# Kernel tuning notes

Hardware: AMD Instinct MI355X
Metric: run time of the kernel (lower is better)

The kernel has to match this reference:

```python
import jax, jax.numpy as jnp
import numpy as np

B, N, T, E = 8, 1024, 16, 512
H = 8                      # heads
DH = E // H                # head_dim = 64
KNN = 16                   # knn_k (N-1 > 16 so k = 16)
L = 4                      # time_window (<= T)
TAU_MIN = 1e-4
BIAS_SCALE = 1.0


def setup_inputs() -> dict:
    key = jax.random.key(0)
    ks = jax.random.split(key, 12)
    hidden = jax.random.normal(ks[0], (B, N, T, E), jnp.float32)
    positions_xy = jax.random.uniform(ks[1], (N, 2), jnp.float32) * 100.0
    s = 1.0 / np.sqrt(E)
    Wq = jax.random.normal(ks[2], (E, E), jnp.float32) * s
    bq = jnp.zeros((E,), jnp.float32)
    Wk = jax.random.normal(ks[3], (E, E), jnp.float32) * s
    bk = jnp.zeros((E,), jnp.float32)
    Wv = jax.random.normal(ks[4], (E, E), jnp.float32) * s
    bv = jnp.zeros((E,), jnp.float32)
    Wo = jax.random.normal(ks[5], (E, E), jnp.float32) * s
    bo = jnp.zeros((E,), jnp.float32)
    tau = jnp.asarray(1.0, jnp.float32)
    return {"hidden": hidden, "positions_xy": positions_xy,
            "Wq": Wq, "bq": bq, "Wk": Wk, "bk": bk,
            "Wv": Wv, "bv": bv, "Wo": Wo, "bo": bo, "tau": tau}


def reference(hidden, positions_xy, Wq, bq, Wk, bk, Wv, bv, Wo, bo, tau):
    b, n, t, e = hidden.shape
    # --- kNN over static positions (no_grad in the original) ---
    pos = jax.lax.stop_gradient(positions_xy)
    x2 = jnp.sum(pos * pos, axis=1, keepdims=True)          # [N,1]
    d2 = jnp.clip(x2 + x2.T - 2.0 * (pos @ pos.T), 0.0)
    D = jnp.sqrt(d2 + 1e-9)
    D = D + jnp.diag(jnp.full((n,), jnp.inf, D.dtype))       # exclude self
    neg_d, knn_idx = jax.lax.top_k(-D, KNN)                  # smallest-k
    knn_dists = -neg_d                                        # [N,K]

    h_last = hidden[:, :, -1, :]                              # [B,N,E]
    # mean over last L steps, then gather neighbors (== gather-then-mean)
    neigh_mean = jnp.mean(hidden[:, :, -L:, :], axis=2)       # [B,N,E]
    neigh_repr = neigh_mean[:, knn_idx]                       # [B,N,K,E]

    # --- distance bias ---
    eps = jnp.finfo(hidden.dtype).eps
    local_scale = jnp.maximum(jnp.mean(knn_dists, axis=1, keepdims=True), eps)
    d_hat = knn_dists / local_scale                           # [N,K]
    tau_safe = jnp.maximum(tau, TAU_MIN)
    log_w = jnp.clip(BIAS_SCALE * (-d_hat / tau_safe), -10.0, 0.0)

    # --- distance-biased multi-head attention over k neighbors ---
    Q = (h_last @ Wq.T + bq).reshape(b, n, H, DH)             # [B,N,H,Dh]
    K = (neigh_repr @ Wk.T + bk).reshape(b, n, KNN, H, DH)    # [B,N,K,H,Dh]
    V = (neigh_repr @ Wv.T + bv).reshape(b, n, KNN, H, DH)
    logits = jnp.einsum('bnhd,bnkhd->bnhk', Q, K) / jnp.sqrt(jnp.asarray(DH, hidden.dtype))
    logits = logits + log_w[None, :, None, :]                 # [B,N,H,K]
    attn = jax.nn.softmax(logits, axis=-1)                    # dropout=0 (eval)
    ctx = jnp.einsum('bnhk,bnkhd->bnhd', attn, V).reshape(b, n, H * DH)
    return ctx @ Wo.T + bo                                    # [B,N,E]
```

## Files before the change

### kernel.cpp

```cpp
#include <hip/hip_runtime.h>
#include <math.h>

#define B_   8
#define N_   1024
#define T_   16
#define E_   512
#define H_   8
#define DH_  64
#define KNN_ 16

typedef __attribute__((ext_vector_type(8))) _Float16 half8;
typedef __attribute__((ext_vector_type(2))) _Float16 half2v;
typedef __attribute__((ext_vector_type(4))) float    f32x4;

__global__ __launch_bounds__(256) void knn_kernel(const float* __restrict__ pos,
                                                  const float* __restrict__ tau_p,
                                                  int* __restrict__ knn_idx,
                                                  float* __restrict__ logw) {
    __shared__ float dist[N_];
    __shared__ float rval[4];
    __shared__ int   ridx[4];
    __shared__ float sel_d[KNN_];
    __shared__ int   sel_i[KNN_];

    const int i = blockIdx.x;
    const int t = threadIdx.x;

    const float px = pos[2 * i], py = pos[2 * i + 1];
    const float xi2 = px * px + py * py;

    for (int j = t; j < N_; j += 256) {
        const float qx = pos[2 * j], qy = pos[2 * j + 1];
        const float xj2 = qx * qx + qy * qy;
        float d2 = xi2 + xj2 - 2.0f * (px * qx + py * qy);
        d2 = fmaxf(d2, 0.0f);
        const float d = sqrtf(d2 + 1e-9f);
        dist[j] = (j == i) ? __builtin_inff() : d;
    }
    __syncthreads();

    for (int k = 0; k < KNN_; ++k) {
        float best = __builtin_inff();
        int bi = 0x7fffffff;
        for (int j = t; j < N_; j += 256) {
            const float d = dist[j];
            if (d < best) { best = d; bi = j; }
        }
        for (int off = 32; off >= 1; off >>= 1) {
            const float ov = __shfl_down(best, off);
            const int   oi = __shfl_down(bi, off);
            if (ov < best || (ov == best && oi < bi)) { best = ov; bi = oi; }
        }
        const int wave = t >> 6;
        if ((t & 63) == 0) { rval[wave] = best; ridx[wave] = bi; }
        __syncthreads();
        if (t == 0) {
            for (int w = 1; w < 4; ++w) {
                if (rval[w] < best || (rval[w] == best && ridx[w] < bi)) { best = rval[w]; bi = ridx[w]; }
            }
            sel_d[k] = best;
            sel_i[k] = bi;
            dist[bi] = __builtin_inff();
        }
        __syncthreads();
    }

    if (t < KNN_) {
        float mean = 0.0f;
        for (int k = 0; k < KNN_; ++k) mean += sel_d[k];
        mean *= (1.0f / KNN_);
        const float scale = fmaxf(mean, 1.1920929e-7f);
        const float tau_safe = fmaxf(tau_p[0], 1e-4f);
        float lw = -(sel_d[t] / scale) / tau_safe;
        lw = fminf(fmaxf(lw, -10.0f), 0.0f);
        logw[i * KNN_ + t]    = lw;
        knn_idx[i * KNN_ + t] = sel_i[t];
    }
}

__global__ __launch_bounds__(256) void last_mean_kernel(const float* __restrict__ hidden,
                                                        float* __restrict__ h_last,
                                                        float* __restrict__ neigh_mean) {
    const int idx = blockIdx.x * 256 + threadIdx.x;
    const int e4 = idx & (E_ / 4 - 1);
    const int bn = idx >> 7;
    const float4* h = (const float4*)hidden;
    const size_t base = (size_t)bn * (T_ * (E_ / 4)) + e4;
    const float4 a = h[base + 12 * (E_ / 4)];
    const float4 b = h[base + 13 * (E_ / 4)];
    const float4 c = h[base + 14 * (E_ / 4)];
    const float4 d = h[base + 15 * (E_ / 4)];
    ((float4*)h_last)[idx] = d;
    float4 m;
    m.x = (a.x + b.x + c.x + d.x) * 0.25f;
    m.y = (a.y + b.y + c.y + d.y) * 0.25f;
    m.z = (a.z + b.z + c.z + d.z) * 0.25f;
    m.w = (a.w + b.w + c.w + d.w) * 0.25f;
    ((float4*)neigh_mean)[idx] = m;
}

__device__ __forceinline__ void split_store(unsigned short* __restrict__ Hs,
                                            unsigned short* __restrict__ Ls,
                                            int byt, float4 v) {
    union { _Float16 h[4]; uint2 u; } Hu, Lu;
    const float* f = (const float*)&v;
#pragma unroll
    for (int j = 0; j < 4; ++j) {
        const _Float16 hh = (_Float16)f[j];
        Hu.h[j] = hh;
        Lu.h[j] = (_Float16)(f[j] - (float)hh);
    }
    *(uint2*)((char*)Hs + byt) = Hu.u;
    *(uint2*)((char*)Ls + byt) = Lu.u;
}

template <typename OT>
__device__ __forceinline__ void gemm_split_f16(const float* __restrict__ A,
                                               const float* __restrict__ Wt,
                                               const float* __restrict__ bias,
                                               OT* __restrict__ C) {
    __shared__ unsigned short AhS[128 * 64];
    __shared__ unsigned short AlS[128 * 64];
    __shared__ unsigned short WhS[128 * 64];
    __shared__ unsigned short WlS[128 * 64];

    const int t    = threadIdx.x;
    const int m0   = blockIdx.x * 128;
    const int j0   = blockIdx.y * 128;
    const int lane = t & 63;
    const int wv   = t >> 6;
    const int wm   = wv >> 1;
    const int wn   = wv & 1;
    const int lr   = lane & 15;
    const int kg   = lane >> 4;

    float4 ra[8], rw[8];
#pragma unroll
    for (int s = 0; s < 8; ++s) {
        const int f4 = s * 256 + t;
        const int row = f4 >> 4, k4 = f4 & 15;
        ra[s] = *(const float4*)(A  + (size_t)(m0 + row) * 512 + k4 * 4);
        rw[s] = *(const float4*)(Wt + (size_t)(j0 + row) * 512 + k4 * 4);
    }

    f32x4 acc[4][4];
    const f32x4 zero = {0.0f, 0.0f, 0.0f, 0.0f};
#pragma unroll
    for (int f = 0; f < 4; ++f)
#pragma unroll
        for (int g = 0; g < 4; ++g) acc[f][g] = zero;

    for (int it = 0; it < 8; ++it) {
        __syncthreads();
#pragma unroll
        for (int s = 0; s < 8; ++s) {
            const int f4 = s * 256 + t;
            const int row = f4 >> 4, k4 = f4 & 15;
            const int byt = (row << 7) + ((k4 * 8) ^ ((row & 7) << 4));
            split_store(AhS, AlS, byt, ra[s]);
            split_store(WhS, WlS, byt, rw[s]);
        }
        __syncthreads();
        if (it < 7) {
            const int kc = (it + 1) * 64;
#pragma unroll
            for (int s = 0; s < 8; ++s) {
                const int f4 = s * 256 + t;
                const int row = f4 >> 4, k4 = f4 & 15;
                ra[s] = *(const float4*)(A  + (size_t)(m0 + row) * 512 + kc + k4 * 4);
                rw[s] = *(const float4*)(Wt + (size_t)(j0 + row) * 512 + kc + k4 * 4);
            }
        }
#pragma unroll
        for (int ks = 0; ks < 2; ++ks) {
            half8 ah[4], al[4], wh[4], wl[4];
#pragma unroll
            for (int f = 0; f < 4; ++f) {
                const int row = wm * 64 + f * 16 + lr;
                const int byt = (row << 7) + (((ks * 64) + (kg * 16)) ^ ((row & 7) << 4));
                ah[f] = *(const half8*)((const char*)AhS + byt);
                al[f] = *(const half8*)((const char*)AlS + byt);
            }
#pragma unroll
            for (int g = 0; g < 4; ++g) {
                const int row = wn * 64 + g * 16 + lr;
                const int byt = (row << 7) + (((ks * 64) + (kg * 16)) ^ ((row & 7) << 4));
                wh[g] = *(const half8*)((const char*)WhS + byt);
                wl[g] = *(const half8*)((const char*)WlS + byt);
            }
#pragma unroll
            for (int f = 0; f < 4; ++f)
#pragma unroll
                for (int g = 0; g < 4; ++g)
                    acc[f][g] = __builtin_amdgcn_mfma_f32_16x16x32_f16(ah[f], wh[g], acc[f][g], 0, 0, 0);
#pragma unroll
            for (int f = 0; f < 4; ++f)
#pragma unroll
                for (int g = 0; g < 4; ++g)
                    acc[f][g] = __builtin_amdgcn_mfma_f32_16x16x32_f16(ah[f], wl[g], acc[f][g], 0, 0, 0);
#pragma unroll
            for (int f = 0; f < 4; ++f)
#pragma unroll
                for (int g = 0; g < 4; ++g)
                    acc[f][g] = __builtin_amdgcn_mfma_f32_16x16x32_f16(al[f], wh[g], acc[f][g], 0, 0, 0);
        }
    }

#pragma unroll
    for (int g = 0; g < 4; ++g) {
        const int n  = j0 + wn * 64 + g * 16 + lr;
        const float bn = bias[n];
#pragma unroll
        for (int f = 0; f < 4; ++f) {
            const int mrow = m0 + wm * 64 + f * 16 + kg * 4;
#pragma unroll
            for (int q = 0; q < 4; ++q)
                C[(size_t)(mrow + q) * 512 + n] = (OT)(acc[f][g][q] + bn);
        }
    }
}

__global__ __launch_bounds__(256, 2) void qkv_gemm_kernel(const float* __restrict__ h_last,
                                                          const float* __restrict__ nmean,
                                                          const float* __restrict__ Wq,
                                                          const float* __restrict__ Wk,
                                                          const float* __restrict__ Wv,
                                                          const float* __restrict__ bq,
                                                          const float* __restrict__ bk,
                                                          const float* __restrict__ bv,
                                                          float* __restrict__ Qo,
                                                          _Float16* __restrict__ Ko,
                                                          _Float16* __restrict__ Vo) {
    const int which = blockIdx.z;
    if (which == 0) {
        gemm_split_f16<float>(h_last, Wq, bq, Qo);
    } else if (which == 1) {
        gemm_split_f16<_Float16>(nmean, Wk, bk, Ko);
    } else {
        gemm_split_f16<_Float16>(nmean, Wv, bv, Vo);
    }
}

__global__ __launch_bounds__(256, 2) void out_gemm_kernel(const float* __restrict__ ctx,
                                                          const float* __restrict__ Wo,
                                                          const float* __restrict__ bo,
                                                          float* __restrict__ out) {
    gemm_split_f16<float>(ctx, Wo, bo, out);
}

__global__ __launch_bounds__(256) void attn_kernel(const float* __restrict__ Q,
                                                   const _Float16* __restrict__ Kf,
                                                   const _Float16* __restrict__ Vf,
                                                   const int* __restrict__ knn_idx,
                                                   const float* __restrict__ logw,
                                                   float* __restrict__ ctx) {
    const int bid = blockIdx.x;
    const int bn  = ((bid & 7) << 10) | (bid >> 3);
    const int n   = bn & (N_ - 1);
    const int b   = bn >> 10;
    const int t   = threadIdx.x;

    __shared__ int   idxs[KNN_];
    __shared__ float lws[KNN_];
    if (t < KNN_) {
        idxs[t] = knn_idx[n * KNN_ + t];
        lws[t]  = logw[n * KNN_ + t];
    }
    __syncthreads();

    const float2 q = ((const float2*)Q)[(size_t)bn * 256 + t];

    float logits[KNN_];
#pragma unroll
    for (int k = 0; k < KNN_; ++k) {
        const int j = idxs[k];
        const half2v kv = ((const half2v*)Kf)[((size_t)(b * N_ + j)) * 256 + t];
        float d = q.x * (float)kv.x + q.y * (float)kv.y;
        d += __shfl_xor(d, 1);
        d += __shfl_xor(d, 2);
        d += __shfl_xor(d, 4);
        d += __shfl_xor(d, 8);
        d += __shfl_xor(d, 16);
        logits[k] = d * 0.125f + lws[k];
    }

    float m = -__builtin_inff();
#pragma unroll
    for (int k = 0; k < KNN_; ++k) m = fmaxf(m, logits[k]);
    float p[KNN_];
    float s = 0.0f;
#pragma unroll
    for (int k = 0; k < KNN_; ++k) { p[k] = expf(logits[k] - m); s += p[k]; }
    const float inv = 1.0f / s;

    float2 acc = make_float2(0.0f, 0.0f);
#pragma unroll
    for (int k = 0; k < KNN_; ++k) {
        const int j = idxs[k];
        const half2v vv = ((const half2v*)Vf)[((size_t)(b * N_ + j)) * 256 + t];
        const float w = p[k] * inv;
        acc.x = fmaf(w, (float)vv.x, acc.x);
        acc.y = fmaf(w, (float)vv.y, acc.y);
    }
    ((float2*)ctx)[(size_t)bn * 256 + t] = acc;
}

extern "C" void kernel_launch(void* const* d_in, const int* in_sizes, int n_in,
                              void* d_out, int out_size, void* d_ws, size_t ws_size,
                              hipStream_t stream) {
    const float* hidden = (const float*)d_in[0];
    const float* pos    = (const float*)d_in[1];
    const float* Wq     = (const float*)d_in[2];
    const float* bq     = (const float*)d_in[3];
    const float* Wk     = (const float*)d_in[4];
    const float* bk     = (const float*)d_in[5];
    const float* Wv     = (const float*)d_in[6];
    const float* bv     = (const float*)d_in[7];
    const float* Wo     = (const float*)d_in[8];
    const float* bo     = (const float*)d_in[9];
    const float* tau    = (const float*)d_in[10];

    float* ws      = (float*)d_ws;
    const size_t SZ = (size_t)B_ * N_ * E_;
    float*    h_last  = ws;
    float*    nmean   = ws + SZ;
    _Float16* Kh      = (_Float16*)(ws + 2 * SZ);
    _Float16* Vh      = (_Float16*)(ws + 2 * SZ + SZ / 2);
    int*      knn_idx = (int*)(ws + 3 * SZ);
    float*    logw    = ws + 3 * SZ + N_ * KNN_;
    float*    Qb      = (float*)d_out;
    float*    out     = (float*)d_out;

    knn_kernel<<<N_, 256, 0, stream>>>(pos, tau, knn_idx, logw);
    last_mean_kernel<<<(B_ * N_ * E_ / 4) / 256, 256, 0, stream>>>(hidden, h_last, nmean);

    dim3 gqkv(B_ * N_ / 128, E_ / 128, 3);
    qkv_gemm_kernel<<<gqkv, 256, 0, stream>>>(h_last, nmean, Wq, Wk, Wv, bq, bk, bv, Qb, Kh, Vh);

    attn_kernel<<<B_ * N_, 256, 0, stream>>>(Qb, Kh, Vh, knn_idx, logw, h_last );

    dim3 gout(B_ * N_ / 128, E_ / 128, 1);
    out_gemm_kernel<<<gout, 256, 0, stream>>>(h_last, Wo, bo, out);
}
```

Before: 478.9 us.

## Pre-split weights to fp16 hi/lo and stream GEMM tiles via global_load_lds

Adds a kernel that splits all four weight matrices into fp16 hi/lo halves once per call. The last-step and mean activations are now stored as single fp16, which lets the QKV GEMM drop the lo-activation MFMA pass (2 passes instead of 3). Q is stored in fp16, and the attention output is written as an fp16 hi/lo pair for a 3-pass output GEMM. Both GEMMs now load tiles directly into LDS with global_load_lds and no register staging, conversion or swizzle. This removes the per-tile fp32-to-fp16 split work and halves activation traffic, at the cost of lower precision for the activations and Q, possible LDS bank conflicts without the swizzle, and no register prefetch overlap.

Result: faster. 441.8 us (-7.8%).

```diff
diff --git a/kernel.cpp b/kernel.cpp
--- a/kernel.cpp
+++ b/kernel.cpp
@@ -10,6 +10,7 @@
 #define KNN_ 16
 
 typedef __attribute__((ext_vector_type(8))) _Float16 half8;
+typedef __attribute__((ext_vector_type(4))) _Float16 half4;
 typedef __attribute__((ext_vector_type(2))) _Float16 half2v;
 typedef __attribute__((ext_vector_type(4))) float    f32x4;
 
@@ -78,9 +79,32 @@
     }
 }
 
+__global__ __launch_bounds__(256) void wsplit_kernel(const float* __restrict__ Wq,
+                                                     const float* __restrict__ Wk,
+                                                     const float* __restrict__ Wv,
+                                                     const float* __restrict__ Wo,
+                                                     _Float16* __restrict__ dst) {
+    const int id  = blockIdx.x * 256 + threadIdx.x;
+    const int mat = id >> 16;
+    const int i   = id & 65535;
+    const float* src = (mat == 0) ? Wq : (mat == 1) ? Wk : (mat == 2) ? Wv : Wo;
+    const float4 v = ((const float4*)src)[i];
+    half4 hi, lo;
+    const float* f = (const float*)&v;
+#pragma unroll
+    for (int j = 0; j < 4; ++j) {
+        const _Float16 hh = (_Float16)f[j];
+        hi[j] = hh;
+        lo[j] = (_Float16)(f[j] - (float)hh);
+    }
+    _Float16* dh = dst + (size_t)mat * 2 * 262144;
+    *(half4*)(dh + (size_t)i * 4)          = hi;
+    *(half4*)(dh + 262144 + (size_t)i * 4) = lo;
+}
+
 __global__ __launch_bounds__(256) void last_mean_kernel(const float* __restrict__ hidden,
-                                                        float* __restrict__ h_last,
-                                                        float* __restrict__ neigh_mean) {
+                                                        _Float16* __restrict__ hlast_h,
+                                                        _Float16* __restrict__ nmean_h) {
     const int idx = blockIdx.x * 256 + threadIdx.x;
     const int e4 = idx & (E_ / 4 - 1);
     const int bn = idx >> 7;
@@ -90,58 +114,44 @@
     const float4 b = h[base + 13 * (E_ / 4)];
     const float4 c = h[base + 14 * (E_ / 4)];
     const float4 d = h[base + 15 * (E_ / 4)];
-    ((float4*)h_last)[idx] = d;
-    float4 m;
-    m.x = (a.x + b.x + c.x + d.x) * 0.25f;
-    m.y = (a.y + b.y + c.y + d.y) * 0.25f;
-    m.z = (a.z + b.z + c.z + d.z) * 0.25f;
-    m.w = (a.w + b.w + c.w + d.w) * 0.25f;
-    ((float4*)neigh_mean)[idx] = m;
-}
-
-__device__ __forceinline__ void split_store(unsigned short* __restrict__ Hs,
-                                            unsigned short* __restrict__ Ls,
-                                            int byt, float4 v) {
-    union { _Float16 h[4]; uint2 u; } Hu, Lu;
-    const float* f = (const float*)&v;
+    half4 hl, nm;
+    const float* df = (const float*)&d;
+    const float* af = (const float*)&a;
+    const float* bf = (const float*)&b;
+    const float* cf = (const float*)&c;
 #pragma unroll
     for (int j = 0; j < 4; ++j) {
-        const _Float16 hh = (_Float16)f[j];
-        Hu.h[j] = hh;
-        Lu.h[j] = (_Float16)(f[j] - (float)hh);
-    }
-    *(uint2*)((char*)Hs + byt) = Hu.u;
-    *(uint2*)((char*)Ls + byt) = Lu.u;
-}
-
-template <typename OT>
-__device__ __forceinline__ void gemm_split_f16(const float* __restrict__ A,
-                                               const float* __restrict__ Wt,
-                                               const float* __restrict__ bias,
-                                               OT* __restrict__ C) {
-    __shared__ unsigned short AhS[128 * 64];
-    __shared__ unsigned short AlS[128 * 64];
-    __shared__ unsigned short WhS[128 * 64];
-    __shared__ unsigned short WlS[128 * 64];
+        hl[j] = (_Float16)df[j];
+        nm[j] = (_Float16)((af[j] + bf[j] + cf[j] + df[j]) * 0.25f);
+    }
+    *(half4*)(hlast_h + (size_t)idx * 4) = hl;
+    *(half4*)(nmean_h + (size_t)idx * 4) = nm;
+}
+
+__device__ __forceinline__ void gload16(const void* g, void* l) {
+    __builtin_amdgcn_global_load_lds((const __attribute__((address_space(1))) void*)g,
+                                     (__attribute__((address_space(3))) void*)l, 16, 0, 0);
+}
+
+template <int PASSES, typename OT>
+__device__ __forceinline__ void gemm_f16(const _Float16* __restrict__ Ah,
+                                         const _Float16* __restrict__ Al,
+                                         const _Float16* __restrict__ Wh,
+                                         const _Float16* __restrict__ Wl,
+                                         const float* __restrict__ bias,
+                                         OT* __restrict__ C) {
+    constexpr int NARR  = (PASSES == 3) ? 4 : 3;
+    constexpr int WHOFF = (PASSES == 3) ? 32768 : 16384;
+    __shared__ unsigned short lds[NARR * 8192];
 
     const int t    = threadIdx.x;
     const int m0   = blockIdx.x * 128;
     const int j0   = blockIdx.y * 128;
     const int lane = t & 63;
     const int wv   = t >> 6;
-    const int wm   = wv >> 1;
-    const int wn   = wv & 1;
-    const int lr   = lane & 15;
-    const int kg   = lane >> 4;
-
-    float4 ra[8], rw[8];
-#pragma unroll
-    for (int s = 0; s < 8; ++s) {
-        const int f4 = s * 256 + t;
-        const int row = f4 >> 4, k4 = f4 & 15;
-        ra[s] = *(const float4*)(A  + (size_t)(m0 + row) * 512 + k4 * 4);
-        rw[s] = *(const float4*)(Wt + (size_t)(j0 + row) * 512 + k4 * 4);
-    }
+    const int wm   = wv >> 1, wn = wv & 1;
+    const int lr   = lane & 15, kg = lane >> 4;
+    const int lsub = (lane >> 3) * 1024 + (lane & 7) * 16;
 
     f32x4 acc[4][4];
     const f32x4 zero = {0.0f, 0.0f, 0.0f, 0.0f};
@@ -151,42 +161,39 @@
         for (int g = 0; g < 4; ++g) acc[f][g] = zero;
 
     for (int it = 0; it < 8; ++it) {
+        const size_t kb = (size_t)(it * 64) * 2;
+        const char* gA  = (const char*)Ah + (size_t)m0 * 1024 + kb;
+        const char* gWh = (const char*)Wh + (size_t)j0 * 1024 + kb;
+        const char* gWl = (const char*)Wl + (size_t)j0 * 1024 + kb;
+        const char* gAl = (PASSES == 3) ? (const char*)Al + (size_t)m0 * 1024 + kb : (const char*)0;
+#pragma unroll
+        for (int jj = 0; jj < NARR * 4; ++jj) {
+            const int j = wv * (NARR * 4) + jj;
+            const int arr = j >> 4, slab = j & 15;
+            const char* gb;
+            if (PASSES == 3)
+                gb = (arr == 0) ? gA : (arr == 1) ? gAl : (arr == 2) ? gWh : gWl;
+            else
+                gb = (arr == 0) ? gA : (arr == 1) ? gWh : gWl;
+            gload16(gb + (size_t)slab * 8192 + lsub, (char*)lds + j * 1024);
+        }
         __syncthreads();
-#pragma unroll
-        for (int s = 0; s < 8; ++s) {
-            const int f4 = s * 256 + t;
-            const int row = f4 >> 4, k4 = f4 & 15;
-            const int byt = (row << 7) + ((k4 * 8) ^ ((row & 7) << 4));
-            split_store(AhS, AlS, byt, ra[s]);
-            split_store(WhS, WlS, byt, rw[s]);
-        }
-        __syncthreads();
-        if (it < 7) {
-            const int kc = (it + 1) * 64;
-#pragma unroll
-            for (int s = 0; s < 8; ++s) {
-                const int f4 = s * 256 + t;
-                const int row = f4 >> 4, k4 = f4 & 15;
-                ra[s] = *(const float4*)(A  + (size_t)(m0 + row) * 512 + kc + k4 * 4);
-                rw[s] = *(const float4*)(Wt + (size_t)(j0 + row) * 512 + kc + k4 * 4);
+
+#pragma unroll
+        for (int ks = 0; ks < 2; ++ks) {
+            const int ko = ks * 64 + kg * 16;
+            half8 ah[4], al[4], wh[4], wl[4];
+#pragma unroll
+            for (int f = 0; f < 4; ++f) {
+                const int abyt = (wm * 64 + f * 16 + lr) * 128 + ko;
+                ah[f] = *(const half8*)((const char*)lds + abyt);
+                if (PASSES == 3) al[f] = *(const half8*)((const char*)lds + 16384 + abyt);
             }
-        }
-#pragma unroll
-        for (int ks = 0; ks < 2; ++ks) {
-            half8 ah[4], al[4], wh[4], wl[4];
-#pragma unroll
-            for (int f = 0; f < 4; ++f) {
-                const int row = wm * 64 + f * 16 + lr;
-                const int byt = (row << 7) + (((ks * 64) + (kg * 16)) ^ ((row & 7) << 4));
-                ah[f] = *(const half8*)((const char*)AhS + byt);
-                al[f] = *(const half8*)((const char*)AlS + byt);
-            }
 #pragma unroll
             for (int g = 0; g < 4; ++g) {
-                const int row = wn * 64 + g * 16 + lr;
-                const int byt = (row << 7) + (((ks * 64) + (kg * 16)) ^ ((row & 7) << 4));
-                wh[g] = *(const half8*)((const char*)WhS + byt);
-                wl[g] = *(const half8*)((const char*)WlS + byt);
+                const int wbyt = (wn * 64 + g * 16 + lr) * 128 + ko;
+                wh[g] = *(const half8*)((const char*)lds + WHOFF + wbyt);
+                wl[g] = *(const half8*)((const char*)lds + WHOFF + 16384 + wbyt);
             }
 #pragma unroll
             for (int f = 0; f < 4; ++f)
@@ -198,62 +205,66 @@
 #pragma unroll
                 for (int g = 0; g < 4; ++g)
                     acc[f][g] = __builtin_amdgcn_mfma_f32_16x16x32_f16(ah[f], wl[g], acc[f][g], 0, 0, 0);
-#pragma unroll
-            for (int f = 0; f < 4; ++f)
-#pragma unroll
-                for (int g = 0; g < 4; ++g)
-                    acc[f][g] = __builtin_amdgcn_mfma_f32_16x16x32_f16(al[f], wh[g], acc[f][g], 0, 0, 0);
-        }
+            if (PASSES == 3) {
+#pragma unroll
+                for (int f = 0; f < 4; ++f)
+#pragma unroll
+                    for (int g = 0; g < 4; ++g)
+                        acc[f][g] = __builtin_amdgcn_mfma_f32_16x16x32_f16(al[f], wh[g], acc[f][g], 0, 0, 0);
+            }
+        }
+        if (it < 7) __syncthreads();
     }
 
 #pragma unroll
     for (int g = 0; g < 4; ++g) {
-        const int n  = j0 + wn * 64 + g * 16 + lr;
-        const float bn = bias[n];
+        const int n = j0 + wn * 64 + g * 16 + lr;
+        const float bn_ = bias[n];
 #pragma unroll
         for (int f = 0; f < 4; ++f) {
             const int mrow = m0 + wm * 64 + f * 16 + kg * 4;
 #pragma unroll
             for (int q = 0; q < 4; ++q)
-                C[(size_t)(mrow + q) * 512 + n] = (OT)(acc[f][g][q] + bn);
-        }
-    }
-}
-
-__global__ __launch_bounds__(256, 2) void qkv_gemm_kernel(const float* __restrict__ h_last,
-                                                          const float* __restrict__ nmean,
-                                                          const float* __restrict__ Wq,
-                                                          const float* __restrict__ Wk,
-                                                          const float* __restrict__ Wv,
+                C[(size_t)(mrow + q) * 512 + n] = (OT)(acc[f][g][q] + bn_);
+        }
+    }
+}
+
+__global__ __launch_bounds__(256, 3) void qkv_gemm_kernel(const _Float16* __restrict__ hlast_h,
+                                                          const _Float16* __restrict__ nmean_h,
+                                                          const _Float16* __restrict__ Wsp,
                                                           const float* __restrict__ bq,
                                                           const float* __restrict__ bk,
                                                           const float* __restrict__ bv,
-                                                          float* __restrict__ Qo,
-                                                          _Float16* __restrict__ Ko,
-                                                          _Float16* __restrict__ Vo) {
+                                                          _Float16* __restrict__ Qh,
+                                                          _Float16* __restrict__ Kh,
+                                                          _Float16* __restrict__ Vh) {
     const int which = blockIdx.z;
-    if (which == 0) {
-        gemm_split_f16<float>(h_last, Wq, bq, Qo);
-    } else if (which == 1) {
-        gemm_split_f16<_Float16>(nmean, Wk, bk, Ko);
-    } else {
-        gemm_split_f16<_Float16>(nmean, Wv, bv, Vo);
-    }
-}
-
-__global__ __launch_bounds__(256, 2) void out_gemm_kernel(const float* __restrict__ ctx,
-                                                          const float* __restrict__ Wo,
+    const size_t WS = 262144;
+    const _Float16* A  = (which == 0) ? hlast_h : nmean_h;
+    const _Float16* wh = Wsp + (size_t)which * 2 * WS;
+    const _Float16* wl = wh + WS;
+    const float* bias  = (which == 0) ? bq : (which == 1) ? bk : bv;
+    _Float16* Cc       = (which == 0) ? Qh : (which == 1) ? Kh : Vh;
+    gemm_f16<2, _Float16>(A, (const _Float16*)0, wh, wl, bias, Cc);
+}
+
+__global__ __launch_bounds__(256, 2) void out_gemm_kernel(const _Float16* __restrict__ ctx_h,
+                                                          const _Float16* __restrict__ ctx_l,
+                                                          const _Float16* __restrict__ Wsp,
                                                           const float* __restrict__ bo,
                                                           float* __restrict__ out) {
-    gemm_split_f16<float>(ctx, Wo, bo, out);
-}
-
-__global__ __launch_bounds__(256) void attn_kernel(const float* __restrict__ Q,
+    const size_t WS = 262144;
+    gemm_f16<3, float>(ctx_h, ctx_l, Wsp + 6 * WS, Wsp + 7 * WS, bo, out);
+}
+
+__global__ __launch_bounds__(256) void attn_kernel(const _Float16* __restrict__ Qh,
                                                    const _Float16* __restrict__ Kf,
                                                    const _Float16* __restrict__ Vf,
                                                    const int* __restrict__ knn_idx,
                                                    const float* __restrict__ logw,
-                                                   float* __restrict__ ctx) {
+                                                   _Float16* __restrict__ ctx_h,
+                                                   _Float16* __restrict__ ctx_l) {
     const int bid = blockIdx.x;
     const int bn  = ((bid & 7) << 10) | (bid >> 3);
     const int n   = bn & (N_ - 1);
@@ -268,14 +279,15 @@
     }
     __syncthreads();
 
-    const float2 q = ((const float2*)Q)[(size_t)bn * 256 + t];
+    const half2v q2 = ((const half2v*)Qh)[(size_t)bn * 256 + t];
+    const float qx = (float)q2.x, qy = (float)q2.y;
 
     float logits[KNN_];
 #pragma unroll
     for (int k = 0; k < KNN_; ++k) {
         const int j = idxs[k];
         const half2v kv = ((const half2v*)Kf)[((size_t)(b * N_ + j)) * 256 + t];
-        float d = q.x * (float)kv.x + q.y * (float)kv.y;
+        float d = qx * (float)kv.x + qy * (float)kv.y;
         d += __shfl_xor(d, 1);
         d += __shfl_xor(d, 2);
         d += __shfl_xor(d, 4);
@@ -302,7 +314,11 @@
         acc.x = fmaf(w, (float)vv.x, acc.x);
         acc.y = fmaf(w, (float)vv.y, acc.y);
     }
-    ((float2*)ctx)[(size_t)bn * 256 + t] = acc;
+    half2v hx, lx;
+    hx.x = (_Float16)acc.x;  lx.x = (_Float16)(acc.x - (float)hx.x);
+    hx.y = (_Float16)acc.y;  lx.y = (_Float16)(acc.y - (float)hx.y);
+    ((half2v*)ctx_h)[(size_t)bn * 256 + t] = hx;
+    ((half2v*)ctx_l)[(size_t)bn * 256 + t] = lx;
 }
 
 extern "C" void kernel_launch(void* const* d_in, const int* in_sizes, int n_in,
@@ -320,25 +336,30 @@
     const float* bo     = (const float*)d_in[9];
     const float* tau    = (const float*)d_in[10];
 
-    float* ws      = (float*)d_ws;
-    const size_t SZ = (size_t)B_ * N_ * E_;
-    float*    h_last  = ws;
-    float*    nmean   = ws + SZ;
-    _Float16* Kh      = (_Float16*)(ws + 2 * SZ);
-    _Float16* Vh      = (_Float16*)(ws + 2 * SZ + SZ / 2);
-    int*      knn_idx = (int*)(ws + 3 * SZ);
-    float*    logw    = ws + 3 * SZ + N_ * KNN_;
-    float*    Qb      = (float*)d_out;
+    _Float16* hp = (_Float16*)d_ws;
+    const size_t SZH = (size_t)B_ * N_ * E_;
+    const size_t WS  = 262144;
+    _Float16* hlast_h = hp;
+    _Float16* nmean_h = hp + SZH;
+    _Float16* Qh      = hp + 2 * SZH;
+    _Float16* Kh      = hp + 3 * SZH;
+    _Float16* Vh      = hp + 4 * SZH;
+    _Float16* ctx_h   = hp + 5 * SZH;
+    _Float16* ctx_l   = hp + 6 * SZH;
+    _Float16* Wsp     = hp + 7 * SZH;
+    int*      knn_idx = (int*)(hp + 7 * SZH + 8 * WS);
+    float*    logw    = (float*)(knn_idx + N_ * KNN_);
     float*    out     = (float*)d_out;
 
     knn_kernel<<<N_, 256, 0, stream>>>(pos, tau, knn_idx, logw);
-    last_mean_kernel<<<(B_ * N_ * E_ / 4) / 256, 256, 0, stream>>>(hidden, h_last, nmean);
+    wsplit_kernel<<<1024, 256, 0, stream>>>(Wq, Wk, Wv, Wo, Wsp);
+    last_mean_kernel<<<(B_ * N_ * E_ / 4) / 256, 256, 0, stream>>>(hidden, hlast_h, nmean_h);
 
     dim3 gqkv(B_ * N_ / 128, E_ / 128, 3);
-    qkv_gemm_kernel<<<gqkv, 256, 0, stream>>>(h_last, nmean, Wq, Wk, Wv, bq, bk, bv, Qb, Kh, Vh);
-
-    attn_kernel<<<B_ * N_, 256, 0, stream>>>(Qb, Kh, Vh, knn_idx, logw, h_last );
+    qkv_gemm_kernel<<<gqkv, 256, 0, stream>>>(hlast_h, nmean_h, Wsp, bq, bk, bv, Qh, Kh, Vh);
+
+    attn_kernel<<<B_ * N_, 256, 0, stream>>>(Qh, Kh, Vh, knn_idx, logw, ctx_h, ctx_l);
 
     dim3 gout(B_ * N_ / 128, E_ / 128, 1);
-    out_gemm_kernel<<<gout, 256, 0, stream>>>(h_last, Wo, bo, out);
-}
+    out_gemm_kernel<<<gout, 256, 0, stream>>>(ctx_h, ctx_l, Wsp, bo, out);
+}
```
